# Kernel optimization log

Measured on AMD Instinct MI355X. Metric: run time of the kernel, lower is better.

Reference implementation:

```python
import math
import jax, jax.numpy as jnp
import numpy as np

B, S, D = 64, 729, 64  # S = (32*14//16 - 1)**2

def setup_inputs() -> dict:
    key = jax.random.key(0)
    kq, kk, kv, km = jax.random.split(key, 4)
    return {
        "query": jax.random.normal(kq, (B, S, D), dtype=jnp.float32),
        "key": jax.random.normal(kk, (B, S, D), dtype=jnp.float32),
        "value": jax.random.normal(kv, (B, S, D), dtype=jnp.float32),
        "mask": jax.random.randint(km, (B, S, S), 0, 2, dtype=jnp.int32),
    }

def reference(query, key, value, mask):
    dk = query.shape[-1]
    # [B,S,S] scores
    scores = jnp.einsum('bqd,bkd->bqk', query, key) / math.sqrt(dk)
    scores = jnp.where(mask == 0, jnp.float32(-1e9), scores)
    attention = jnp.tanh(scores)  # args.activation == 'tanh'
    # ignore_diag == 1: zero the diagonal of each [S,S] attention map
    eye = jnp.eye(attention.shape[-1], dtype=attention.dtype)
    attention = attention * (1.0 - eye)
    out = jnp.einsum('bqk,bkd->bqd', attention, value)
    return (out, attention)
```

## Files before the change

### kernel.cpp

```cpp
#include <hip/hip_runtime.h>

#define BATCH 64
#define SEQ 729
#define DIM 64
#define QT 12
#define NKT 12
#define KSPLIT 2
#define KT (NKT / KSPLIT)
#define STRB 72
#define MSTR 68
#define OSTR 68

typedef __attribute__((ext_vector_type(8))) short bf16x8;
typedef __attribute__((ext_vector_type(4))) float f32x4;
typedef int   i32x4a __attribute__((ext_vector_type(4), aligned(4)));
typedef float f32x4a __attribute__((ext_vector_type(4), aligned(4)));

__device__ __forceinline__ unsigned short f2bf(float f) {
    unsigned int u = __float_as_uint(f);
    u += 0x7fffu + ((u >> 16) & 1u);
    return (unsigned short)(u >> 16);
}

__device__ __forceinline__ unsigned long long pack4bf(float a, float b, float c, float d) {
    return (unsigned long long)f2bf(a)
         | ((unsigned long long)f2bf(b) << 16)
         | ((unsigned long long)f2bf(c) << 32)
         | ((unsigned long long)f2bf(d) << 48);
}

__device__ __forceinline__ float bf2f(unsigned int hi16) {
    return __uint_as_float(hi16 << 16);
}

__device__ __forceinline__ float fast_tanh(float x) {
    float e = __builtin_amdgcn_exp2f(x * 2.88539008177792681f);
    return 1.0f - 2.0f * __builtin_amdgcn_rcpf(e + 1.0f);
}

#define BAR() do { \
    asm volatile("s_waitcnt lgkmcnt(0)" ::: "memory"); \
    __builtin_amdgcn_s_barrier(); \
    __builtin_amdgcn_sched_barrier(0); \
} while (0)

__global__ __launch_bounds__(256, 3) void attn_kernel(
    const float* __restrict__ Qg, const float* __restrict__ Kg,
    const float* __restrict__ Vg, const int* __restrict__ Mg,
    float* __restrict__ Og, float* __restrict__ Ag)
{
    __shared__ __align__(16) unsigned char smem[32000];
    unsigned short* Ks  = (unsigned short*)(smem);
    unsigned short* Vs  = (unsigned short*)(smem + 9216);
    unsigned short* Qs  = (unsigned short*)(smem + 18432);
    unsigned char*  Mb8 = smem + 27648;
    float* Ostage = (float*)smem;

    const int tid = threadIdx.x;
    const int q0  = blockIdx.x * 64;
    const int b   = blockIdx.y;
    const int kt0 = blockIdx.z * KT;

    const float* Qb = Qg + (size_t)b * SEQ * DIM;
    const float* Kb = Kg + (size_t)b * SEQ * DIM;
    const float* Vb = Vg + (size_t)b * SEQ * DIM;
    const int*   Mb = Mg + (size_t)b * SEQ * SEQ;
    float* Ob = Og + (size_t)b * SEQ * DIM;
    float* Ab = Ag + (size_t)b * SEQ * SEQ;

    const int lane = tid & 63;
    const int quad = lane >> 4;
    const int l15  = lane & 15;
    const int qrow = (tid >> 6) * 16;

    const int rr = tid >> 4;
    const int cc = (tid & 15) * 4;
    const int vd0 = (tid & 15) * 4;
    const int vk0 = (tid >> 4) * 4;
    const int prow = qrow + (lane >> 4);
    const int pcol = (lane & 15) * 4;

    float4 kr[4], vr[4];
    i32x4a mr[4];

    auto load_k = [&](int k0n) {
        #pragma unroll
        for (int i = 0; i < 4; ++i) {
            int gk = k0n + rr + 16 * i;
            kr[i] = (gk < SEQ) ? *(const float4*)(Kb + gk * DIM + cc)
                               : float4{0, 0, 0, 0};
        }
    };
    auto load_v = [&](int k0n) {
        #pragma unroll
        for (int i = 0; i < 4; ++i) {
            int gk = k0n + vk0 + i;
            vr[i] = (gk < SEQ) ? *(const float4*)(Vb + gk * DIM + vd0)
                               : float4{0, 0, 0, 0};
        }
    };
    auto load_mask = [&](int k0n) {
        #pragma unroll
        for (int i = 0; i < 4; ++i) {
            int gq = q0 + prow + 4 * i;
            int gk = k0n + pcol;
            if (gq < SEQ && gk + 3 < SEQ) {
                mr[i] = *(const i32x4a*)(Mb + (size_t)gq * SEQ + gk);
            } else if (gq < SEQ) {
                i32x4a t;
                #pragma unroll
                for (int e = 0; e < 4; ++e)
                    t[e] = (gk + e < SEQ) ? Mb[(size_t)gq * SEQ + gk + e] : 0;
                mr[i] = t;
            } else {
                mr[i] = i32x4a{0, 0, 0, 0};
            }
        }
    };
    auto drain_mask = [&]() {
        #pragma unroll
        for (int i = 0; i < 4; ++i) {
            unsigned int mb = (unsigned)(mr[i][0] & 1)
                            | ((unsigned)(mr[i][1] & 1) << 8)
                            | ((unsigned)(mr[i][2] & 1) << 16)
                            | ((unsigned)(mr[i][3] & 1) << 24);
            *(unsigned int*)&Mb8[(prow + 4 * i) * MSTR + pcol] = mb;
        }
    };
    auto drain_kv = [&]() {
        #pragma unroll
        for (int i = 0; i < 4; ++i)
            *(unsigned long long*)&Ks[(rr + 16 * i) * STRB + cc] =
                pack4bf(kr[i].x, kr[i].y, kr[i].z, kr[i].w);
        #pragma unroll
        for (int j = 0; j < 4; ++j) {
            float v0 = j==0?vr[0].x:j==1?vr[0].y:j==2?vr[0].z:vr[0].w;
            float v1 = j==0?vr[1].x:j==1?vr[1].y:j==2?vr[1].z:vr[1].w;
            float v2 = j==0?vr[2].x:j==1?vr[2].y:j==2?vr[2].z:vr[2].w;
            float v3 = j==0?vr[3].x:j==1?vr[3].y:j==2?vr[3].z:vr[3].w;
            *(unsigned long long*)&Vs[(vd0 + j) * STRB + vk0] = pack4bf(v0, v1, v2, v3);
        }
    };

    #pragma unroll
    for (int i = 0; i < 4; ++i) {
        int gq = q0 + rr + 16 * i;
        float4 x = (gq < SEQ) ? *(const float4*)(Qb + gq * DIM + cc)
                              : float4{0, 0, 0, 0};
        *(unsigned long long*)&Qs[(rr + 16 * i) * STRB + cc] = pack4bf(x.x, x.y, x.z, x.w);
    }
    BAR();

    const bf16x8 aq0 = *(const bf16x8*)&Qs[(qrow + l15) * STRB + quad * 8];
    const bf16x8 aq1 = *(const bf16x8*)&Qs[(qrow + l15) * STRB + 32 + quad * 8];

    load_k(kt0 * 64); load_v(kt0 * 64); load_mask(kt0 * 64);

    f32x4 oacc[4];
    #pragma unroll
    for (int dt = 0; dt < 4; ++dt) {
        oacc[dt][0]=0.f; oacc[dt][1]=0.f; oacc[dt][2]=0.f; oacc[dt][3]=0.f;
    }

    for (int t = 0; t < KT; ++t) {
        const int k0 = (kt0 + t) * 64;

        BAR();
        drain_mask();
        drain_kv();
        BAR();

        if (t + 1 < KT) {
            load_k(k0 + 64); load_v(k0 + 64); load_mask(k0 + 64);
        }

        f32x4 sacc[4];
        #pragma unroll
        for (int n = 0; n < 4; ++n) {
            bf16x8 bk0 = *(const bf16x8*)&Ks[(n * 16 + l15) * STRB + quad * 8];
            bf16x8 bk1 = *(const bf16x8*)&Ks[(n * 16 + l15) * STRB + 32 + quad * 8];
            f32x4 c; c[0]=0.f; c[1]=0.f; c[2]=0.f; c[3]=0.f;
            c = __builtin_amdgcn_mfma_f32_16x16x32_bf16(aq0, bk0, c, 0, 0, 0);
            c = __builtin_amdgcn_mfma_f32_16x16x32_bf16(aq1, bk1, c, 0, 0, 0);
            sacc[n] = c;
        }

        #pragma unroll
        for (int n = 0; n < 4; ++n) {
            int col = n * 16 + l15;
            int gk  = k0 + col;
            #pragma unroll
            for (int r = 0; r < 4; ++r) {
                int qloc = qrow + quad * 4 + r;
                int gq = q0 + qloc;
                int m = Mb8[qloc * MSTR + col];
                float sv = sacc[n][r] * 0.125f;
                bool msk = (m == 0);
                float p = fast_tanh(msk ? -1e9f : sv);
                if (msk) p = -1.0f;
                if (gq == gk) p = 0.0f;
                if (gq >= SEQ || gk >= SEQ) p = 0.0f;
                Qs[qloc * STRB + col] = f2bf(p);
            }
        }

        #pragma unroll
        for (int i = 0; i < 4; ++i) {
            int row = prow + 4 * i;
            int gq  = q0 + row;
            int gk  = k0 + pcol;
            unsigned long long w = *(const unsigned long long*)&Qs[row * STRB + pcol];
            f32x4 pv;
            pv[0] = bf2f((unsigned)(w      ) & 0xffffu);
            pv[1] = bf2f((unsigned)(w >> 16) & 0xffffu);
            pv[2] = bf2f((unsigned)(w >> 32) & 0xffffu);
            pv[3] = bf2f((unsigned)(w >> 48) & 0xffffu);
            if (gq < SEQ) {
                if (gk + 3 < SEQ) {
                    *(f32x4a*)(Ab + (size_t)gq * SEQ + gk) = pv;
                } else {
                    #pragma unroll
                    for (int e = 0; e < 4; ++e)
                        if (gk + e < SEQ) Ab[(size_t)gq * SEQ + gk + e] = pv[e];
                }
            }
        }

        const bf16x8 ap0 = *(const bf16x8*)&Qs[(qrow + l15) * STRB + quad * 8];
        const bf16x8 ap1 = *(const bf16x8*)&Qs[(qrow + l15) * STRB + 32 + quad * 8];
        #pragma unroll
        for (int dt = 0; dt < 4; ++dt) {
            bf16x8 bv0 = *(const bf16x8*)&Vs[(dt * 16 + l15) * STRB + quad * 8];
            bf16x8 bv1 = *(const bf16x8*)&Vs[(dt * 16 + l15) * STRB + 32 + quad * 8];
            oacc[dt] = __builtin_amdgcn_mfma_f32_16x16x32_bf16(ap0, bv0, oacc[dt], 0, 0, 0);
            oacc[dt] = __builtin_amdgcn_mfma_f32_16x16x32_bf16(ap1, bv1, oacc[dt], 0, 0, 0);
        }
    }

    BAR();
    #pragma unroll
    for (int dt = 0; dt < 4; ++dt)
        #pragma unroll
        for (int r = 0; r < 4; ++r)
            Ostage[(qrow + quad * 4 + r) * OSTR + dt * 16 + l15] = oacc[dt][r];
    #pragma unroll
    for (int r16 = 0; r16 < 16; ++r16) {
        int row = qrow + r16;
        int gq  = q0 + row;
        float val = Ostage[row * OSTR + lane];
        if (gq < SEQ)
            atomicAdd(Ob + (size_t)gq * DIM + lane, val);
    }
}

extern "C" void kernel_launch(void* const* d_in, const int* in_sizes, int n_in,
                              void* d_out, int out_size, void* d_ws, size_t ws_size,
                              hipStream_t stream) {
    const float* Q = (const float*)d_in[0];
    const float* K = (const float*)d_in[1];
    const float* V = (const float*)d_in[2];
    const int*   M = (const int*)d_in[3];
    float* Out  = (float*)d_out;
    float* Attn = Out + (size_t)BATCH * SEQ * DIM;
    hipMemsetAsync(Out, 0, (size_t)BATCH * SEQ * DIM * sizeof(float), stream);
    dim3 grid(QT, BATCH, KSPLIT);
    attn_kernel<<<grid, 256, 0, stream>>>(Q, K, V, M, Out, Attn);
}
```

Measured before the change: 336.3 us.

## Drop K-split atomics and double-buffer K/V tiles in shared memory

Each block now walks all 12 key tiles itself instead of splitting keys across two blocks. This removes the output memset and the per-element atomicAdd reduction, and the output is written with plain vector stores. K and V get ping-pong LDS buffers, so the next tile is staged while the current one is consumed, leaving one barrier per iteration instead of two. The P·V MMA now runs before the attention-map store, and the mask/tanh logic is simplified. The cost is about 50KB of LDS per block and half as many blocks, which could limit occupancy or latency hiding.

```diff
diff --git a/kernel.cpp b/kernel.cpp
--- a/kernel.cpp
+++ b/kernel.cpp
@@ -3,10 +3,7 @@
 #define BATCH 64
 #define SEQ 729
 #define DIM 64
-#define QT 12
-#define NKT 12
-#define KSPLIT 2
-#define KT (NKT / KSPLIT)
+#define NT 12
 #define STRB 72
 #define MSTR 68
 #define OSTR 68
@@ -49,17 +46,18 @@
     const float* __restrict__ Vg, const int* __restrict__ Mg,
     float* __restrict__ Og, float* __restrict__ Ag)
 {
-    __shared__ __align__(16) unsigned char smem[32000];
-    unsigned short* Ks  = (unsigned short*)(smem);
-    unsigned short* Vs  = (unsigned short*)(smem + 9216);
-    unsigned short* Qs  = (unsigned short*)(smem + 18432);
-    unsigned char*  Mb8 = smem + 27648;
+    __shared__ __align__(16) unsigned char smem[50432];
+    unsigned short* Ks0 = (unsigned short*)(smem);
+    unsigned short* Vs0 = (unsigned short*)(smem + 9216);
+    unsigned short* Ks1 = (unsigned short*)(smem + 18432);
+    unsigned short* Vs1 = (unsigned short*)(smem + 27648);
+    unsigned short* Ps  = (unsigned short*)(smem + 36864);
+    unsigned char*  Mb8 = smem + 46080;
     float* Ostage = (float*)smem;
 
     const int tid = threadIdx.x;
     const int q0  = blockIdx.x * 64;
     const int b   = blockIdx.y;
-    const int kt0 = blockIdx.z * KT;
 
     const float* Qb = Qg + (size_t)b * SEQ * DIM;
     const float* Kb = Kg + (size_t)b * SEQ * DIM;
@@ -127,10 +125,10 @@
             *(unsigned int*)&Mb8[(prow + 4 * i) * MSTR + pcol] = mb;
         }
     };
-    auto drain_kv = [&]() {
+    auto drain_kv = [&](unsigned short* Kd, unsigned short* Vd) {
         #pragma unroll
         for (int i = 0; i < 4; ++i)
-            *(unsigned long long*)&Ks[(rr + 16 * i) * STRB + cc] =
+            *(unsigned long long*)&Kd[(rr + 16 * i) * STRB + cc] =
                 pack4bf(kr[i].x, kr[i].y, kr[i].z, kr[i].w);
         #pragma unroll
         for (int j = 0; j < 4; ++j) {
@@ -138,23 +136,27 @@
             float v1 = j==0?vr[1].x:j==1?vr[1].y:j==2?vr[1].z:vr[1].w;
             float v2 = j==0?vr[2].x:j==1?vr[2].y:j==2?vr[2].z:vr[2].w;
             float v3 = j==0?vr[3].x:j==1?vr[3].y:j==2?vr[3].z:vr[3].w;
-            *(unsigned long long*)&Vs[(vd0 + j) * STRB + vk0] = pack4bf(v0, v1, v2, v3);
-        }
-    };
-
+            *(unsigned long long*)&Vd[(vd0 + j) * STRB + vk0] = pack4bf(v0, v1, v2, v3);
+        }
+    };
+
+    load_k(0); load_v(0); load_mask(0);
     #pragma unroll
     for (int i = 0; i < 4; ++i) {
         int gq = q0 + rr + 16 * i;
         float4 x = (gq < SEQ) ? *(const float4*)(Qb + gq * DIM + cc)
                               : float4{0, 0, 0, 0};
-        *(unsigned long long*)&Qs[(rr + 16 * i) * STRB + cc] = pack4bf(x.x, x.y, x.z, x.w);
+        *(unsigned long long*)&Ps[(rr + 16 * i) * STRB + cc] = pack4bf(x.x, x.y, x.z, x.w);
     }
     BAR();
 
-    const bf16x8 aq0 = *(const bf16x8*)&Qs[(qrow + l15) * STRB + quad * 8];
-    const bf16x8 aq1 = *(const bf16x8*)&Qs[(qrow + l15) * STRB + 32 + quad * 8];
-
-    load_k(kt0 * 64); load_v(kt0 * 64); load_mask(kt0 * 64);
+    const bf16x8 aq0 = *(const bf16x8*)&Ps[(qrow + l15) * STRB + quad * 8];
+    const bf16x8 aq1 = *(const bf16x8*)&Ps[(qrow + l15) * STRB + 32 + quad * 8];
+
+    drain_mask();
+    drain_kv(Ks0, Vs0);
+    load_k(64); load_v(64); load_mask(64);
+    BAR();
 
     f32x4 oacc[4];
     #pragma unroll
@@ -162,23 +164,18 @@
         oacc[dt][0]=0.f; oacc[dt][1]=0.f; oacc[dt][2]=0.f; oacc[dt][3]=0.f;
     }
 
-    for (int t = 0; t < KT; ++t) {
-        const int k0 = (kt0 + t) * 64;
-
-        BAR();
-        drain_mask();
-        drain_kv();
-        BAR();
-
-        if (t + 1 < KT) {
-            load_k(k0 + 64); load_v(k0 + 64); load_mask(k0 + 64);
-        }
+    for (int t = 0; t < NT; ++t) {
+        const int k0 = t * 64;
+        const unsigned short* KsC = (t & 1) ? Ks1 : Ks0;
+        const unsigned short* VsC = (t & 1) ? Vs1 : Vs0;
+        unsigned short* KsN = (t & 1) ? Ks0 : Ks1;
+        unsigned short* VsN = (t & 1) ? Vs0 : Vs1;
 
         f32x4 sacc[4];
         #pragma unroll
         for (int n = 0; n < 4; ++n) {
-            bf16x8 bk0 = *(const bf16x8*)&Ks[(n * 16 + l15) * STRB + quad * 8];
-            bf16x8 bk1 = *(const bf16x8*)&Ks[(n * 16 + l15) * STRB + 32 + quad * 8];
+            bf16x8 bk0 = *(const bf16x8*)&KsC[(n * 16 + l15) * STRB + quad * 8];
+            bf16x8 bk1 = *(const bf16x8*)&KsC[(n * 16 + l15) * STRB + 32 + quad * 8];
             f32x4 c; c[0]=0.f; c[1]=0.f; c[2]=0.f; c[3]=0.f;
             c = __builtin_amdgcn_mfma_f32_16x16x32_bf16(aq0, bk0, c, 0, 0, 0);
             c = __builtin_amdgcn_mfma_f32_16x16x32_bf16(aq1, bk1, c, 0, 0, 0);
@@ -195,13 +192,20 @@
                 int gq = q0 + qloc;
                 int m = Mb8[qloc * MSTR + col];
                 float sv = sacc[n][r] * 0.125f;
-                bool msk = (m == 0);
-                float p = fast_tanh(msk ? -1e9f : sv);
-                if (msk) p = -1.0f;
-                if (gq == gk) p = 0.0f;
-                if (gq >= SEQ || gk >= SEQ) p = 0.0f;
-                Qs[qloc * STRB + col] = f2bf(p);
-            }
+                float p = fast_tanh((m == 0) ? -1e9f : sv);
+                if (gq == gk || gk >= SEQ) p = 0.0f;
+                Ps[qloc * STRB + col] = f2bf(p);
+            }
+        }
+
+        const bf16x8 ap0 = *(const bf16x8*)&Ps[(qrow + l15) * STRB + quad * 8];
+        const bf16x8 ap1 = *(const bf16x8*)&Ps[(qrow + l15) * STRB + 32 + quad * 8];
+        #pragma unroll
+        for (int dt = 0; dt < 4; ++dt) {
+            bf16x8 bv0 = *(const bf16x8*)&VsC[(dt * 16 + l15) * STRB + quad * 8];
+            bf16x8 bv1 = *(const bf16x8*)&VsC[(dt * 16 + l15) * STRB + 32 + quad * 8];
+            oacc[dt] = __builtin_amdgcn_mfma_f32_16x16x32_bf16(ap0, bv0, oacc[dt], 0, 0, 0);
+            oacc[dt] = __builtin_amdgcn_mfma_f32_16x16x32_bf16(ap1, bv1, oacc[dt], 0, 0, 0);
         }
 
         #pragma unroll
@@ -209,7 +213,7 @@
             int row = prow + 4 * i;
             int gq  = q0 + row;
             int gk  = k0 + pcol;
-            unsigned long long w = *(const unsigned long long*)&Qs[row * STRB + pcol];
+            unsigned long long w = *(const unsigned long long*)&Ps[row * STRB + pcol];
             f32x4 pv;
             pv[0] = bf2f((unsigned)(w      ) & 0xffffu);
             pv[1] = bf2f((unsigned)(w >> 16) & 0xffffu);
@@ -226,14 +230,13 @@
             }
         }
 
-        const bf16x8 ap0 = *(const bf16x8*)&Qs[(qrow + l15) * STRB + quad * 8];
-        const bf16x8 ap1 = *(const bf16x8*)&Qs[(qrow + l15) * STRB + 32 + quad * 8];
-        #pragma unroll
-        for (int dt = 0; dt < 4; ++dt) {
-            bf16x8 bv0 = *(const bf16x8*)&Vs[(dt * 16 + l15) * STRB + quad * 8];
-            bf16x8 bv1 = *(const bf16x8*)&Vs[(dt * 16 + l15) * STRB + 32 + quad * 8];
-            oacc[dt] = __builtin_amdgcn_mfma_f32_16x16x32_bf16(ap0, bv0, oacc[dt], 0, 0, 0);
-            oacc[dt] = __builtin_amdgcn_mfma_f32_16x16x32_bf16(ap1, bv1, oacc[dt], 0, 0, 0);
+        if (t + 1 < NT) {
+            drain_mask();
+            drain_kv(KsN, VsN);
+            if (t + 2 < NT) {
+                load_k(k0 + 128); load_v(k0 + 128); load_mask(k0 + 128);
+            }
+            BAR();
         }
     }
 
@@ -244,12 +247,11 @@
         for (int r = 0; r < 4; ++r)
             Ostage[(qrow + quad * 4 + r) * OSTR + dt * 16 + l15] = oacc[dt][r];
     #pragma unroll
-    for (int r16 = 0; r16 < 16; ++r16) {
-        int row = qrow + r16;
+    for (int i = 0; i < 4; ++i) {
+        int row = prow + 4 * i;
         int gq  = q0 + row;
-        float val = Ostage[row * OSTR + lane];
-        if (gq < SEQ)
-            atomicAdd(Ob + (size_t)gq * DIM + lane, val);
+        f32x4 ov = *(const f32x4*)&Ostage[row * OSTR + pcol];
+        if (gq < SEQ) *(f32x4*)(Ob + (size_t)gq * DIM + pcol) = ov;
     }
 }
 
@@ -262,7 +264,6 @@
     const int*   M = (const int*)d_in[3];
     float* Out  = (float*)d_out;
     float* Attn = Out + (size_t)BATCH * SEQ * DIM;
-    hipMemsetAsync(Out, 0, (size_t)BATCH * SEQ * DIM * sizeof(float), stream);
-    dim3 grid(QT, BATCH, KSPLIT);
+    dim3 grid(NT, BATCH);
     attn_kernel<<<grid, 256, 0, stream>>>(Q, K, V, M, Out, Attn);
 }
```

New measurement: 324.9 us. -3.4%, faster.
